# Kernel optimization log

Measured on AMD Instinct MI355X. Metric: run time of the kernel, lower is better.

## Reference

```python
import jax, jax.numpy as jnp
import numpy as np

NUM_HEADS = 8
AREA = 4
EPS = 1e-5  # torch BatchNorm2d default


def _conv1x1(x, w):
    # x: [B,C,H,W], w: [O,C] -> [B,O,H,W]
    return jnp.einsum('bchw,oc->bohw', x, w)


def _bn(y, g, b, m, v):
    # inference-mode BatchNorm2d, per-channel affine
    s = g / jnp.sqrt(v + EPS)
    return y * s[None, :, None, None] + (b - m * s)[None, :, None, None]


def setup_inputs() -> dict:
    key = jax.random.key(0)
    ks = jax.random.split(key, 16)
    B, C, H, W = 2, 256, 64, 64
    d = {}
    d['x'] = jax.random.normal(ks[0], (B, C, H, W), jnp.float32)
    # qk conv (dim -> 2*dim) + BN
    d['w_qk'] = jax.random.normal(ks[1], (2 * C, C), jnp.float32) * 0.06
    d['g_qk'] = jax.random.uniform(ks[2], (2 * C,), jnp.float32, 0.5, 1.5)
    d['b_qk'] = jax.random.normal(ks[3], (2 * C,), jnp.float32) * 0.1
    d['m_qk'] = jax.random.normal(ks[4], (2 * C,), jnp.float32) * 0.1
    d['v_qk'] = jax.random.uniform(ks[5], (2 * C,), jnp.float32, 0.5, 1.5)
    # v conv (dim -> dim) + BN
    d['w_v'] = jax.random.normal(ks[6], (C, C), jnp.float32) * 0.06
    d['g_v'] = jax.random.uniform(ks[7], (C,), jnp.float32, 0.5, 1.5)
    d['b_v'] = jax.random.normal(ks[8], (C,), jnp.float32) * 0.1
    d['m_v'] = jax.random.normal(ks[9], (C,), jnp.float32) * 0.1
    d['v_v'] = jax.random.uniform(ks[10], (C,), jnp.float32, 0.5, 1.5)
    # proj conv (dim -> dim) + BN
    d['w_p'] = jax.random.normal(ks[11], (C, C), jnp.float32) * 0.06
    d['g_p'] = jax.random.uniform(ks[12], (C,), jnp.float32, 0.5, 1.5)
    d['b_p'] = jax.random.normal(ks[13], (C,), jnp.float32) * 0.1
    d['m_p'] = jax.random.normal(ks[14], (C,), jnp.float32) * 0.1
    d['v_p'] = jax.random.uniform(ks[15], (C,), jnp.float32, 0.5, 1.5)
    return d


def reference(x, w_qk, g_qk, b_qk, m_qk, v_qk,
              w_v, g_v, b_v, m_v, v_v,
              w_p, g_p, b_p, m_p, v_p):
    B, C, H, W = x.shape
    N = H * W
    hd = C // NUM_HEADS

    qk = _bn(_conv1x1(x, w_qk), g_qk, b_qk, m_qk, v_qk)          # [B,2C,H,W]
    qk = qk.reshape(B, 2 * C, N).transpose(0, 2, 1)               # [B,N,2C]
    vv = _bn(_conv1x1(x, w_v), g_v, b_v, m_v, v_v)                # [B,C,H,W]
    vv = vv.reshape(B, C, N).transpose(0, 2, 1)                   # [B,N,C]

    Ba, Na = B * AREA, N // AREA
    qk = qk.reshape(Ba, Na, 2 * C)
    vv = vv.reshape(Ba, Na, C)
    q, k = qk[..., :C], qk[..., C:]

    # [Ba,Na,C] -> [Ba,heads,hd,Na] (matches torch transpose(1,2).view)
    q = q.reshape(Ba, Na, NUM_HEADS, hd).transpose(0, 2, 3, 1)
    k = k.reshape(Ba, Na, NUM_HEADS, hd).transpose(0, 2, 3, 1)
    v = vv.reshape(Ba, Na, NUM_HEADS, hd).transpose(0, 2, 3, 1)

    scale = hd ** -0.5
    attn = jnp.einsum('bhdi,bhdj->bhij', q, k) * scale            # [Ba,h,Na,Na]
    attn = jax.nn.softmax(attn, axis=-1)                          # max-sub exp/sum
    out = jnp.einsum('bhdj,bhij->bihd', v, attn)                  # [Ba,Na,h,hd]

    out = out.reshape(B, N, C).reshape(B, H, W, C).transpose(0, 3, 1, 2)
    return _bn(_conv1x1(out, w_p), g_p, b_p, m_p, v_p)            # [B,C,H,W]
```

## Files before the change

kernel.cpp:

```cpp
#include <hip/hip_runtime.h>
#include <hip/hip_bf16.h>
#include <math.h>

#define CCH   256
#define NPIX  4096
#define NHD   8
#define HD    32
#define NA    1024
#define BN_EPS 1e-5f
#define ATT_SCALE (0.17677669529663687f * 1.4426950408889634f)

typedef __attribute__((ext_vector_type(8))) short bf16x8;
typedef __attribute__((ext_vector_type(4))) short bf16x4;
typedef __attribute__((ext_vector_type(4))) float f32x4;

static __device__ inline short f2bf(float f) {
    union { float f; unsigned u; } v; v.f = f;
    unsigned r = (v.u + 0x7fff + ((v.u >> 16) & 1)) >> 16;
    return (short)r;
}

static __device__ inline unsigned int pk2bf(float a, float b) {
    __hip_bfloat162 h2 = __float22bfloat162_rn(make_float2(a, b));
    union { __hip_bfloat162 h; unsigned int u; } v; v.h = h2;
    return v.u;
}

__global__ __launch_bounds__(256)
void prep_kernel(const float* __restrict__ x, short* __restrict__ Xt,
                 const float* __restrict__ wqk, const float* __restrict__ wv,
                 const float* __restrict__ wp, short* __restrict__ Wb) {
    __shared__ short tile[64][66];
    const int t = threadIdx.x;
    const int z = blockIdx.z;
    if (z == 2) {
        const int id  = blockIdx.y * 64 + blockIdx.x;
        const int idx = (id * 256 + t) * 4;
        const float* src; int off;
        if (idx < 131072)      { src = wqk; off = idx; }
        else if (idx < 196608) { src = wv;  off = idx - 131072; }
        else                   { src = wp;  off = idx - 196608; }
        const float4 v = *(const float4*)(src + off);
        short4 o;
        o.x = f2bf(v.x); o.y = f2bf(v.y); o.z = f2bf(v.z); o.w = f2bf(v.w);
        *(short4*)(Wb + idx) = o;
        return;
    }
    const int n0 = blockIdx.x << 6;
    const int c0 = blockIdx.y << 6;
    const int b  = z;
    const float* xp = x + (((size_t)(b * CCH + c0)) << 12) + n0;
    #pragma unroll
    for (int j = 0; j < 16; ++j) {
        const int lin = (j << 8) + t;
        const int cl = lin >> 6, nl = lin & 63;
        tile[cl][nl] = f2bf(xp[((size_t)cl << 12) + nl]);
    }
    __syncthreads();
    short* xtp = Xt + ((((size_t)b << 12) + n0) << 8) + c0;
    #pragma unroll
    for (int j = 0; j < 16; ++j) {
        const int lin = (j << 8) + t;
        const int nl = lin >> 6, cl = lin & 63;
        xtp[((size_t)nl << 8) + cl] = tile[cl][nl];
    }
}

__global__ __launch_bounds__(256)
void qkv_gemm(const short* __restrict__ Xt, const short* __restrict__ Wb,
              const float* __restrict__ g_qk, const float* __restrict__ b_qk,
              const float* __restrict__ m_qk, const float* __restrict__ v_qk,
              const float* __restrict__ g_v, const float* __restrict__ b_v,
              const float* __restrict__ m_v, const float* __restrict__ v_v,
              short* __restrict__ Qb, short* __restrict__ Kb,
              short* __restrict__ Vb) {
    __shared__ short A_lds[64][72];
    __shared__ short B_lds[64][72];
    const int t    = threadIdx.x;
    const int lane = t & 63;
    const int w    = t >> 6;
    const int c    = lane & 15;
    const int quad = lane >> 4;
    const int wm   = w >> 1;
    const int wn   = w & 1;
    const int m0 = blockIdx.x * 64;
    const int n0 = blockIdx.y * 64;

    const int rowS = t >> 3;
    const int kc   = t & 7;
    const short* gA0 = Xt + (size_t)(m0 + rowS) * 256 + kc * 8;
    const short* gA1 = gA0 + 32 * 256;
    const short* gB0 = Wb + (size_t)(n0 + rowS) * 256 + kc * 8;
    const short* gB1 = gB0 + 32 * 256;
    short* lA0 = &A_lds[rowS][kc * 8];
    short* lA1 = &A_lds[rowS + 32][kc * 8];
    short* lB0 = &B_lds[rowS][kc * 8];
    short* lB1 = &B_lds[rowS + 32][kc * 8];

    f32x4 acc[2][2];
    #pragma unroll
    for (int f = 0; f < 2; ++f)
        #pragma unroll
        for (int g = 0; g < 2; ++g) acc[f][g] = (f32x4){0.f, 0.f, 0.f, 0.f};

    #pragma unroll
    for (int kt = 0; kt < 4; ++kt) {
        const int k0 = kt * 64;
        bf16x8 a0 = *(const bf16x8*)(gA0 + k0);
        bf16x8 a1 = *(const bf16x8*)(gA1 + k0);
        bf16x8 b0 = *(const bf16x8*)(gB0 + k0);
        bf16x8 b1 = *(const bf16x8*)(gB1 + k0);
        if (kt) __syncthreads();
        *(bf16x8*)lA0 = a0;
        *(bf16x8*)lA1 = a1;
        *(bf16x8*)lB0 = b0;
        *(bf16x8*)lB1 = b1;
        __syncthreads();
        #pragma unroll
        for (int s = 0; s < 2; ++s) {
            const int ko = s * 32 + quad * 8;
            bf16x8 af0 = *(const bf16x8*)&A_lds[wm * 32 + c][ko];
            bf16x8 af1 = *(const bf16x8*)&A_lds[wm * 32 + 16 + c][ko];
            bf16x8 bg0 = *(const bf16x8*)&B_lds[wn * 32 + c][ko];
            bf16x8 bg1 = *(const bf16x8*)&B_lds[wn * 32 + 16 + c][ko];
            acc[0][0] = __builtin_amdgcn_mfma_f32_16x16x32_bf16(af0, bg0, acc[0][0], 0, 0, 0);
            acc[0][1] = __builtin_amdgcn_mfma_f32_16x16x32_bf16(af0, bg1, acc[0][1], 0, 0, 0);
            acc[1][0] = __builtin_amdgcn_mfma_f32_16x16x32_bf16(af1, bg0, acc[1][0], 0, 0, 0);
            acc[1][1] = __builtin_amdgcn_mfma_f32_16x16x32_bf16(af1, bg1, acc[1][1], 0, 0, 0);
        }
    }

    const int mw = m0 + wm * 32;
    const int nw = n0 + wn * 32;
    if (n0 < 512) {
        const bool isQ = (n0 < 256);
        short* dst = isQ ? Qb : Kb;
        const float fold = isQ ? ATT_SCALE : 1.0f;
        #pragma unroll
        for (int g = 0; g < 2; ++g) {
            const int o  = nw + g * 16 + c;
            const int cd = o & 255;
            const int h  = cd >> 5;
            const int d  = cd & 31;
            float s    = g_qk[o] * rsqrtf(v_qk[o] + BN_EPS);
            float beta = (b_qk[o] - m_qk[o] * s) * fold;
            s *= fold;
            #pragma unroll
            for (int f = 0; f < 2; ++f) {
                #pragma unroll
                for (int r = 0; r < 4; ++r) {
                    const int row  = mw + f * 16 + (quad << 2) + r;
                    const int pair = (row >> 10) * NHD + h;
                    const int i    = row & 1023;
                    dst[(((size_t)pair << 10) + i) * HD + d] = f2bf(acc[f][g][r] * s + beta);
                }
            }
        }
    } else {
        #pragma unroll
        for (int g = 0; g < 2; ++g) {
            const int c2 = nw + g * 16 + c - 512;
            const int d  = c2 & 31;
            const int hp = c2 >> 5;
            const float s    = g_v[c2] * rsqrtf(v_v[c2] + BN_EPS);
            const float beta = b_v[c2] - m_v[c2] * s;
            #pragma unroll
            for (int f = 0; f < 2; ++f) {
                #pragma unroll
                for (int r = 0; r < 4; ++r) {
                    const int row  = mw + f * 16 + (quad << 2) + r;
                    const int pair = (row >> 10) * NHD + hp;
                    const int j    = row & 1023;
                    Vb[((size_t)pair << 15) + (d << 10) + j] = f2bf(acc[f][g][r] * s + beta);
                }
            }
        }
    }
}

__global__ __launch_bounds__(256, 4)
void attn_kernel(const short* __restrict__ Qb,
                 const short* __restrict__ Kb,
                 const short* __restrict__ Vb,
                 short* __restrict__ AOt) {
    const int tid  = threadIdx.x;
    const int wave = tid >> 6;
    const int lane = tid & 63;
    const int c    = lane & 15;
    const int quad = lane >> 4;
    const int pidx  = wave >> 1;
    const int jhalf = wave & 1;

    const int bx  = blockIdx.x;
    const int hi  = bx >> 3;
    const int p   = (bx & 7) + ((hi >> 4) << 3);
    const int blk = hi & 15;
    const int i0a = (blk << 6) + (pidx << 5);
    const int i0b = i0a + 16;
    const int ba  = p >> 3;
    const int h   = p & 7;

    __shared__ f32x4 mrgA[2][4][64];
    __shared__ float mrgL[2][2][64];

    const short* qbase = Qb + ((size_t)p << 15);
    const short* kbase = Kb + ((size_t)p << 15);
    const short* vbase = Vb + ((size_t)p << 15);

    bf16x8 qfa = *(const bf16x8*)(qbase + ((i0a + c) << 5) + (quad << 3));
    bf16x8 qfb = *(const bf16x8*)(qbase + ((i0b + c) << 5) + (quad << 3));

    const int perm = ((c >> 2) << 3) + (c & 3);
    const short* kp0 = kbase + (perm << 5) + (quad << 3);
    const short* kp1 = kp0 + 128;
    const short* vp0 = vbase + (c << 10) + (quad << 3);
    const short* vp1 = vbase + ((c + 16) << 10) + (quad << 3);

    f32x4 acc0a = {0.f,0.f,0.f,0.f}, acc1a = {0.f,0.f,0.f,0.f};
    f32x4 acc0b = {0.f,0.f,0.f,0.f}, acc1b = {0.f,0.f,0.f,0.f};
    float la = 0.f, lb = 0.f;
    const f32x4 zero = {0.f,0.f,0.f,0.f};

    const int jbeg = jhalf << 9;
    for (int jj = 0; jj < 512; jj += 32) {
        const int j0 = jbeg + jj;
        bf16x8 kf0 = *(const bf16x8*)(kp0 + (j0 << 5));
        bf16x8 kf1 = *(const bf16x8*)(kp1 + (j0 << 5));
        bf16x8 vf0 = *(const bf16x8*)(vp0 + j0);
        bf16x8 vf1 = *(const bf16x8*)(vp1 + j0);

        f32x4 s0a = __builtin_amdgcn_mfma_f32_16x16x32_bf16(kf0, qfa, zero, 0, 0, 0);
        f32x4 s1a = __builtin_amdgcn_mfma_f32_16x16x32_bf16(kf1, qfa, zero, 0, 0, 0);
        f32x4 s0b = __builtin_amdgcn_mfma_f32_16x16x32_bf16(kf0, qfb, zero, 0, 0, 0);
        f32x4 s1b = __builtin_amdgcn_mfma_f32_16x16x32_bf16(kf1, qfb, zero, 0, 0, 0);

        float p0a[4], p1a[4], p0b[4], p1b[4];
        #pragma unroll
        for (int r = 0; r < 4; ++r) {
            p0a[r] = __builtin_amdgcn_exp2f(s0a[r]);
            p1a[r] = __builtin_amdgcn_exp2f(s1a[r]);
            p0b[r] = __builtin_amdgcn_exp2f(s0b[r]);
            p1b[r] = __builtin_amdgcn_exp2f(s1b[r]);
        }
        la += (p0a[0]+p0a[1]) + (p0a[2]+p0a[3]) + (p1a[0]+p1a[1]) + (p1a[2]+p1a[3]);
        lb += (p0b[0]+p0b[1]) + (p0b[2]+p0b[3]) + (p1b[0]+p1b[1]) + (p1b[2]+p1b[3]);

        union { unsigned int u[4]; bf16x8 v; } pfa, pfb;
        pfa.u[0] = pk2bf(p0a[0], p0a[1]);
        pfa.u[1] = pk2bf(p0a[2], p0a[3]);
        pfa.u[2] = pk2bf(p1a[0], p1a[1]);
        pfa.u[3] = pk2bf(p1a[2], p1a[3]);
        pfb.u[0] = pk2bf(p0b[0], p0b[1]);
        pfb.u[1] = pk2bf(p0b[2], p0b[3]);
        pfb.u[2] = pk2bf(p1b[0], p1b[1]);
        pfb.u[3] = pk2bf(p1b[2], p1b[3]);

        acc0a = __builtin_amdgcn_mfma_f32_16x16x32_bf16(pfa.v, vf0, acc0a, 0, 0, 0);
        acc1a = __builtin_amdgcn_mfma_f32_16x16x32_bf16(pfa.v, vf1, acc1a, 0, 0, 0);
        acc0b = __builtin_amdgcn_mfma_f32_16x16x32_bf16(pfb.v, vf0, acc0b, 0, 0, 0);
        acc1b = __builtin_amdgcn_mfma_f32_16x16x32_bf16(pfb.v, vf1, acc1b, 0, 0, 0);
    }

    if (jhalf == 1) {
        mrgA[pidx][0][lane] = acc0a;
        mrgA[pidx][1][lane] = acc1a;
        mrgA[pidx][2][lane] = acc0b;
        mrgA[pidx][3][lane] = acc1b;
        mrgL[pidx][0][lane] = la;
        mrgL[pidx][1][lane] = lb;
    }
    __syncthreads();
    if (jhalf == 1) return;

    acc0a += mrgA[pidx][0][lane];
    acc1a += mrgA[pidx][1][lane];
    acc0b += mrgA[pidx][2][lane];
    acc1b += mrgA[pidx][3][lane];
    la += mrgL[pidx][0][lane];
    lb += mrgL[pidx][1][lane];

    la += __shfl_xor(la, 16); la += __shfl_xor(la, 32);
    lb += __shfl_xor(lb, 16); lb += __shfl_xor(lb, 32);

    #pragma unroll
    for (int r = 0; r < 4; ++r) {
        const int rr = (quad << 2) + r;
        const float rla = 1.f / __shfl(la, rr, 16);
        const float rlb = 1.f / __shfl(lb, rr, 16);
        const size_t basea = ((((size_t)ba << 10) + i0a + rr) << 8) + (h << 5);
        const size_t baseb = ((((size_t)ba << 10) + i0b + rr) << 8) + (h << 5);
        AOt[basea + c]      = f2bf(acc0a[r] * rla);
        AOt[basea + c + 16] = f2bf(acc1a[r] * rla);
        AOt[baseb + c]      = f2bf(acc0b[r] * rlb);
        AOt[baseb + c + 16] = f2bf(acc1b[r] * rlb);
    }
}

__global__ __launch_bounds__(256)
void pconv_gemm(const short* __restrict__ Wp, const short* __restrict__ AOt,
                const float* __restrict__ g_p, const float* __restrict__ b_p,
                const float* __restrict__ m_p, const float* __restrict__ v_p,
                float* __restrict__ out) {
    __shared__ short A_lds[64][72];
    __shared__ short B_lds[64][72];
    const int t    = threadIdx.x;
    const int lane = t & 63;
    const int w    = t >> 6;
    const int c    = lane & 15;
    const int quad = lane >> 4;
    const int wm   = w >> 1;
    const int wn   = w & 1;
    const int m0 = blockIdx.x * 64;
    const int n0 = blockIdx.y * 64;

    const int rowS = t >> 3;
    const int kc   = t & 7;
    const short* gA0 = Wp + (size_t)(m0 + rowS) * 256 + kc * 8;
    const short* gA1 = gA0 + 32 * 256;
    const short* gB0 = AOt + (size_t)(n0 + rowS) * 256 + kc * 8;
    const short* gB1 = gB0 + 32 * 256;
    short* lA0 = &A_lds[rowS][kc * 8];
    short* lA1 = &A_lds[rowS + 32][kc * 8];
    short* lB0 = &B_lds[rowS][kc * 8];
    short* lB1 = &B_lds[rowS + 32][kc * 8];

    f32x4 acc[2][2];
    #pragma unroll
    for (int f = 0; f < 2; ++f)
        #pragma unroll
        for (int g = 0; g < 2; ++g) acc[f][g] = (f32x4){0.f, 0.f, 0.f, 0.f};

    #pragma unroll
    for (int kt = 0; kt < 4; ++kt) {
        const int k0 = kt * 64;
        bf16x8 a0 = *(const bf16x8*)(gA0 + k0);
        bf16x8 a1 = *(const bf16x8*)(gA1 + k0);
        bf16x8 b0 = *(const bf16x8*)(gB0 + k0);
        bf16x8 b1 = *(const bf16x8*)(gB1 + k0);
        if (kt) __syncthreads();
        *(bf16x8*)lA0 = a0;
        *(bf16x8*)lA1 = a1;
        *(bf16x8*)lB0 = b0;
        *(bf16x8*)lB1 = b1;
        __syncthreads();
        #pragma unroll
        for (int s = 0; s < 2; ++s) {
            const int ko = s * 32 + quad * 8;
            bf16x8 af0 = *(const bf16x8*)&A_lds[wm * 32 + c][ko];
            bf16x8 af1 = *(const bf16x8*)&A_lds[wm * 32 + 16 + c][ko];
            bf16x8 bg0 = *(const bf16x8*)&B_lds[wn * 32 + c][ko];
            bf16x8 bg1 = *(const bf16x8*)&B_lds[wn * 32 + 16 + c][ko];
            acc[0][0] = __builtin_amdgcn_mfma_f32_16x16x32_bf16(af0, bg0, acc[0][0], 0, 0, 0);
            acc[0][1] = __builtin_amdgcn_mfma_f32_16x16x32_bf16(af0, bg1, acc[0][1], 0, 0, 0);
            acc[1][0] = __builtin_amdgcn_mfma_f32_16x16x32_bf16(af1, bg0, acc[1][0], 0, 0, 0);
            acc[1][1] = __builtin_amdgcn_mfma_f32_16x16x32_bf16(af1, bg1, acc[1][1], 0, 0, 0);
        }
    }

    const int mw = m0 + wm * 32;
    const int nw = n0 + wn * 32;
    #pragma unroll
    for (int f = 0; f < 2; ++f) {
        #pragma unroll
        for (int r = 0; r < 4; ++r) {
            const int o = mw + f * 16 + (quad << 2) + r;
            const float s    = g_p[o] * rsqrtf(v_p[o] + BN_EPS);
            const float beta = b_p[o] - m_p[o] * s;
            #pragma unroll
            for (int g = 0; g < 2; ++g) {
                const int col = nw + g * 16 + c;
                const int b = col >> 12, n = col & 4095;
                out[((size_t)(b * CCH + o) << 12) + n] = acc[f][g][r] * s + beta;
            }
        }
    }
}

extern "C" void kernel_launch(void* const* d_in, const int* in_sizes, int n_in,
                              void* d_out, int out_size, void* d_ws, size_t ws_size,
                              hipStream_t stream) {
    const float* x    = (const float*)d_in[0];
    const float* w_qk = (const float*)d_in[1];
    const float* g_qk = (const float*)d_in[2];
    const float* b_qk = (const float*)d_in[3];
    const float* m_qk = (const float*)d_in[4];
    const float* v_qk = (const float*)d_in[5];
    const float* w_v  = (const float*)d_in[6];
    const float* g_v  = (const float*)d_in[7];
    const float* b_v  = (const float*)d_in[8];
    const float* m_v  = (const float*)d_in[9];
    const float* v_v  = (const float*)d_in[10];
    const float* w_p  = (const float*)d_in[11];
    const float* g_p  = (const float*)d_in[12];
    const float* b_p  = (const float*)d_in[13];
    const float* m_p  = (const float*)d_in[14];
    const float* v_p  = (const float*)d_in[15];

    short* Qb  = (short*)d_ws;
    short* Kb  = Qb + 2097152;
    short* Vb  = Kb + 2097152;
    short* Xt  = Vb + 2097152;
    short* Wb  = Xt + 2097152;
    short* AOt = Xt;

    dim3 gprep(64, 4, 3);
    prep_kernel<<<gprep, 256, 0, stream>>>(x, Xt, w_qk, w_v, w_p, Wb);

    dim3 gqkv(128, 12);
    qkv_gemm<<<gqkv, 256, 0, stream>>>(Xt, Wb, g_qk, b_qk, m_qk, v_qk,
                                       g_v, b_v, m_v, v_v, Qb, Kb, Vb);

    attn_kernel<<<1024, 256, 0, stream>>>(Qb, Kb, Vb, AOt);

    dim3 gp(4, 128);
    pconv_gemm<<<gp, 256, 0, stream>>>(Wb + 768 * 256, AOt, g_p, b_p, m_p, v_p, (float*)d_out);
}
```

Before: 132.1 us.

## Split attention key range across four waves per 32-row query block

Each block now handles 32 query rows, with all four waves splitting the 1024 keys into quarters. Previously two waves each covered half the keys for 64 rows. The grid doubles to 2048 blocks and launch bounds rise to 6 blocks per SM, aiming at more parallelism and shorter per-wave loops. The cost is a three-way shared-memory merge in which three of four waves idle after the barrier, plus more Q reloads and partial-sum traffic.

```diff
diff --git a/kernel.cpp b/kernel.cpp
--- a/kernel.cpp
+++ b/kernel.cpp
@@ -178,7 +178,7 @@
     }
 }
 
-__global__ __launch_bounds__(256, 4)
+__global__ __launch_bounds__(256, 6)
 void attn_kernel(const short* __restrict__ Qb,
                  const short* __restrict__ Kb,
                  const short* __restrict__ Vb,
@@ -188,20 +188,18 @@
     const int lane = tid & 63;
     const int c    = lane & 15;
     const int quad = lane >> 4;
-    const int pidx  = wave >> 1;
-    const int jhalf = wave & 1;
-
-    const int bx  = blockIdx.x;
-    const int hi  = bx >> 3;
-    const int p   = (bx & 7) + ((hi >> 4) << 3);
-    const int blk = hi & 15;
-    const int i0a = (blk << 6) + (pidx << 5);
+
+    const int bx = blockIdx.x;
+    const int hi = bx >> 3;
+    const int p  = ((hi >> 5) << 3) | (bx & 7);
+    const int ig = hi & 31;
+    const int i0a = ig << 5;
     const int i0b = i0a + 16;
     const int ba  = p >> 3;
     const int h   = p & 7;
 
-    __shared__ f32x4 mrgA[2][4][64];
-    __shared__ float mrgL[2][2][64];
+    __shared__ f32x4 mrgA[3][4][64];
+    __shared__ float mrgL[3][2][64];
 
     const short* qbase = Qb + ((size_t)p << 15);
     const short* kbase = Kb + ((size_t)p << 15);
@@ -221,8 +219,8 @@
     float la = 0.f, lb = 0.f;
     const f32x4 zero = {0.f,0.f,0.f,0.f};
 
-    const int jbeg = jhalf << 9;
-    for (int jj = 0; jj < 512; jj += 32) {
+    const int jbeg = wave << 8;
+    for (int jj = 0; jj < 256; jj += 32) {
         const int j0 = jbeg + jj;
         bf16x8 kf0 = *(const bf16x8*)(kp0 + (j0 << 5));
         bf16x8 kf1 = *(const bf16x8*)(kp1 + (j0 << 5));
@@ -261,23 +259,26 @@
         acc1b = __builtin_amdgcn_mfma_f32_16x16x32_bf16(pfb.v, vf1, acc1b, 0, 0, 0);
     }
 
-    if (jhalf == 1) {
-        mrgA[pidx][0][lane] = acc0a;
-        mrgA[pidx][1][lane] = acc1a;
-        mrgA[pidx][2][lane] = acc0b;
-        mrgA[pidx][3][lane] = acc1b;
-        mrgL[pidx][0][lane] = la;
-        mrgL[pidx][1][lane] = lb;
+    if (wave > 0) {
+        mrgA[wave - 1][0][lane] = acc0a;
+        mrgA[wave - 1][1][lane] = acc1a;
+        mrgA[wave - 1][2][lane] = acc0b;
+        mrgA[wave - 1][3][lane] = acc1b;
+        mrgL[wave - 1][0][lane] = la;
+        mrgL[wave - 1][1][lane] = lb;
     }
     __syncthreads();
-    if (jhalf == 1) return;
-
-    acc0a += mrgA[pidx][0][lane];
-    acc1a += mrgA[pidx][1][lane];
-    acc0b += mrgA[pidx][2][lane];
-    acc1b += mrgA[pidx][3][lane];
-    la += mrgL[pidx][0][lane];
-    lb += mrgL[pidx][1][lane];
+    if (wave > 0) return;
+
+    #pragma unroll
+    for (int q = 0; q < 3; ++q) {
+        acc0a += mrgA[q][0][lane];
+        acc1a += mrgA[q][1][lane];
+        acc0b += mrgA[q][2][lane];
+        acc1b += mrgA[q][3][lane];
+        la += mrgL[q][0][lane];
+        lb += mrgL[q][1][lane];
+    }
 
     la += __shfl_xor(la, 16); la += __shfl_xor(la, 32);
     lb += __shfl_xor(lb, 16); lb += __shfl_xor(lb, 32);
@@ -410,7 +411,7 @@
     qkv_gemm<<<gqkv, 256, 0, stream>>>(Xt, Wb, g_qk, b_qk, m_qk, v_qk,
                                        g_v, b_v, m_v, v_v, Qb, Kb, Vb);
 
-    attn_kernel<<<1024, 256, 0, stream>>>(Qb, Kb, Vb, AOt);
+    attn_kernel<<<2048, 256, 0, stream>>>(Qb, Kb, Vb, AOt);
 
     dim3 gp(4, 128);
     pconv_gemm<<<gp, 256, 0, stream>>>(Wb + 768 * 256, AOt, g_p, b_p, m_p, v_p, (float*)d_out);
```

Result: no change. 133.4 us (+0.9%).

## Stage K/V tiles in LDS for attention and enlarge QKV GEMM M-tile

Applied to the files above, without the earlier changes.

The attention kernel now loads K and V tiles for both j-halves into shared memory with coalesced cooperative loads, and applies the row permutation at load time. Before, each wave read K and V fragments straight from global memory. The QKV GEMM moves to a 128-row M-tile so each wave computes 64x32 with 8 accumulators, halving the grid and reusing B fragments more. This adds block-wide syncs in the attention loop and more registers and LDS per block, which could cut occupancy.

```diff
diff --git a/kernel.cpp b/kernel.cpp
--- a/kernel.cpp
+++ b/kernel.cpp
@@ -74,7 +74,7 @@
               const float* __restrict__ m_v, const float* __restrict__ v_v,
               short* __restrict__ Qb, short* __restrict__ Kb,
               short* __restrict__ Vb) {
-    __shared__ short A_lds[64][72];
+    __shared__ short A_lds[128][72];
     __shared__ short B_lds[64][72];
     const int t    = threadIdx.x;
     const int lane = t & 63;
@@ -83,23 +83,27 @@
     const int quad = lane >> 4;
     const int wm   = w >> 1;
     const int wn   = w & 1;
-    const int m0 = blockIdx.x * 64;
-    const int n0 = blockIdx.y * 64;
+    const int m0 = blockIdx.x * 128;
+    const int n0 = blockIdx.y * 64 + wn * 32;
 
     const int rowS = t >> 3;
     const int kc   = t & 7;
     const short* gA0 = Xt + (size_t)(m0 + rowS) * 256 + kc * 8;
     const short* gA1 = gA0 + 32 * 256;
-    const short* gB0 = Wb + (size_t)(n0 + rowS) * 256 + kc * 8;
+    const short* gA2 = gA0 + 64 * 256;
+    const short* gA3 = gA0 + 96 * 256;
+    const short* gB0 = Wb + (size_t)(blockIdx.y * 64 + rowS) * 256 + kc * 8;
     const short* gB1 = gB0 + 32 * 256;
     short* lA0 = &A_lds[rowS][kc * 8];
     short* lA1 = &A_lds[rowS + 32][kc * 8];
+    short* lA2 = &A_lds[rowS + 64][kc * 8];
+    short* lA3 = &A_lds[rowS + 96][kc * 8];
     short* lB0 = &B_lds[rowS][kc * 8];
     short* lB1 = &B_lds[rowS + 32][kc * 8];
 
-    f32x4 acc[2][2];
-    #pragma unroll
-    for (int f = 0; f < 2; ++f)
+    f32x4 acc[4][2];
+    #pragma unroll
+    for (int f = 0; f < 4; ++f)
         #pragma unroll
         for (int g = 0; g < 2; ++g) acc[f][g] = (f32x4){0.f, 0.f, 0.f, 0.f};
 
@@ -108,37 +112,44 @@
         const int k0 = kt * 64;
         bf16x8 a0 = *(const bf16x8*)(gA0 + k0);
         bf16x8 a1 = *(const bf16x8*)(gA1 + k0);
+        bf16x8 a2 = *(const bf16x8*)(gA2 + k0);
+        bf16x8 a3 = *(const bf16x8*)(gA3 + k0);
         bf16x8 b0 = *(const bf16x8*)(gB0 + k0);
         bf16x8 b1 = *(const bf16x8*)(gB1 + k0);
         if (kt) __syncthreads();
         *(bf16x8*)lA0 = a0;
         *(bf16x8*)lA1 = a1;
+        *(bf16x8*)lA2 = a2;
+        *(bf16x8*)lA3 = a3;
         *(bf16x8*)lB0 = b0;
         *(bf16x8*)lB1 = b1;
         __syncthreads();
         #pragma unroll
         for (int s = 0; s < 2; ++s) {
             const int ko = s * 32 + quad * 8;
-            bf16x8 af0 = *(const bf16x8*)&A_lds[wm * 32 + c][ko];
-            bf16x8 af1 = *(const bf16x8*)&A_lds[wm * 32 + 16 + c][ko];
-            bf16x8 bg0 = *(const bf16x8*)&B_lds[wn * 32 + c][ko];
-            bf16x8 bg1 = *(const bf16x8*)&B_lds[wn * 32 + 16 + c][ko];
-            acc[0][0] = __builtin_amdgcn_mfma_f32_16x16x32_bf16(af0, bg0, acc[0][0], 0, 0, 0);
-            acc[0][1] = __builtin_amdgcn_mfma_f32_16x16x32_bf16(af0, bg1, acc[0][1], 0, 0, 0);
-            acc[1][0] = __builtin_amdgcn_mfma_f32_16x16x32_bf16(af1, bg0, acc[1][0], 0, 0, 0);
-            acc[1][1] = __builtin_amdgcn_mfma_f32_16x16x32_bf16(af1, bg1, acc[1][1], 0, 0, 0);
-        }
-    }
-
-    const int mw = m0 + wm * 32;
-    const int nw = n0 + wn * 32;
+            bf16x8 af[4], bg[2];
+            #pragma unroll
+            for (int f = 0; f < 4; ++f)
+                af[f] = *(const bf16x8*)&A_lds[wm * 64 + f * 16 + c][ko];
+            #pragma unroll
+            for (int g = 0; g < 2; ++g)
+                bg[g] = *(const bf16x8*)&B_lds[wn * 32 + g * 16 + c][ko];
+            #pragma unroll
+            for (int f = 0; f < 4; ++f)
+                #pragma unroll
+                for (int g = 0; g < 2; ++g)
+                    acc[f][g] = __builtin_amdgcn_mfma_f32_16x16x32_bf16(af[f], bg[g], acc[f][g], 0, 0, 0);
+        }
+    }
+
+    const int mw = m0 + wm * 64;
     if (n0 < 512) {
         const bool isQ = (n0 < 256);
         short* dst = isQ ? Qb : Kb;
         const float fold = isQ ? ATT_SCALE : 1.0f;
         #pragma unroll
         for (int g = 0; g < 2; ++g) {
-            const int o  = nw + g * 16 + c;
+            const int o  = n0 + g * 16 + c;
             const int cd = o & 255;
             const int h  = cd >> 5;
             const int d  = cd & 31;
@@ -146,7 +157,7 @@
             float beta = (b_qk[o] - m_qk[o] * s) * fold;
             s *= fold;
             #pragma unroll
-            for (int f = 0; f < 2; ++f) {
+            for (int f = 0; f < 4; ++f) {
                 #pragma unroll
                 for (int r = 0; r < 4; ++r) {
                     const int row  = mw + f * 16 + (quad << 2) + r;
@@ -159,13 +170,13 @@
     } else {
         #pragma unroll
         for (int g = 0; g < 2; ++g) {
-            const int c2 = nw + g * 16 + c - 512;
+            const int c2 = n0 + g * 16 + c - 512;
             const int d  = c2 & 31;
             const int hp = c2 >> 5;
             const float s    = g_v[c2] * rsqrtf(v_v[c2] + BN_EPS);
             const float beta = b_v[c2] - m_v[c2] * s;
             #pragma unroll
-            for (int f = 0; f < 2; ++f) {
+            for (int f = 0; f < 4; ++f) {
                 #pragma unroll
                 for (int r = 0; r < 4; ++r) {
                     const int row  = mw + f * 16 + (quad << 2) + r;
@@ -200,6 +211,8 @@
     const int ba  = p >> 3;
     const int h   = p & 7;
 
+    __shared__ __align__(16) short Klds[2][64][40];
+    __shared__ __align__(16) short Vlds[2][32][72];
     __shared__ f32x4 mrgA[2][4][64];
     __shared__ float mrgL[2][2][64];
 
@@ -210,57 +223,80 @@
     bf16x8 qfa = *(const bf16x8*)(qbase + ((i0a + c) << 5) + (quad << 3));
     bf16x8 qfb = *(const bf16x8*)(qbase + ((i0b + c) << 5) + (quad << 3));
 
-    const int perm = ((c >> 2) << 3) + (c & 3);
-    const short* kp0 = kbase + (perm << 5) + (quad << 3);
-    const short* kp1 = kp0 + 128;
-    const short* vp0 = vbase + (c << 10) + (quad << 3);
-    const short* vp1 = vbase + ((c + 16) << 10) + (quad << 3);
+    const int krow = tid >> 2;
+    const int kkc  = tid & 3;
+    const int jj_  = krow >> 5;
+    const int r32  = krow & 31;
+    const int r16  = r32 & 15;
+    const int srcr = ((r16 >> 2) << 3) + (r16 & 3) + ((r32 >> 4) << 2) + (jj_ << 5);
+    const short* kS = kbase + (srcr << 5) + kkc * 8;
+    short* kD0 = &Klds[0][krow][kkc * 8];
+    short* kD1 = &Klds[1][krow][kkc * 8];
+    const int vrow = tid >> 3;
+    const int vkc  = tid & 7;
+    const short* vS = vbase + (vrow << 10) + vkc * 8;
+    short* vD0 = &Vlds[0][vrow][vkc * 8];
+    short* vD1 = &Vlds[1][vrow][vkc * 8];
 
     f32x4 acc0a = {0.f,0.f,0.f,0.f}, acc1a = {0.f,0.f,0.f,0.f};
     f32x4 acc0b = {0.f,0.f,0.f,0.f}, acc1b = {0.f,0.f,0.f,0.f};
     float la = 0.f, lb = 0.f;
     const f32x4 zero = {0.f,0.f,0.f,0.f};
 
-    const int jbeg = jhalf << 9;
-    for (int jj = 0; jj < 512; jj += 32) {
-        const int j0 = jbeg + jj;
-        bf16x8 kf0 = *(const bf16x8*)(kp0 + (j0 << 5));
-        bf16x8 kf1 = *(const bf16x8*)(kp1 + (j0 << 5));
-        bf16x8 vf0 = *(const bf16x8*)(vp0 + j0);
-        bf16x8 vf1 = *(const bf16x8*)(vp1 + j0);
-
-        f32x4 s0a = __builtin_amdgcn_mfma_f32_16x16x32_bf16(kf0, qfa, zero, 0, 0, 0);
-        f32x4 s1a = __builtin_amdgcn_mfma_f32_16x16x32_bf16(kf1, qfa, zero, 0, 0, 0);
-        f32x4 s0b = __builtin_amdgcn_mfma_f32_16x16x32_bf16(kf0, qfb, zero, 0, 0, 0);
-        f32x4 s1b = __builtin_amdgcn_mfma_f32_16x16x32_bf16(kf1, qfb, zero, 0, 0, 0);
-
-        float p0a[4], p1a[4], p0b[4], p1b[4];
-        #pragma unroll
-        for (int r = 0; r < 4; ++r) {
-            p0a[r] = __builtin_amdgcn_exp2f(s0a[r]);
-            p1a[r] = __builtin_amdgcn_exp2f(s1a[r]);
-            p0b[r] = __builtin_amdgcn_exp2f(s0b[r]);
-            p1b[r] = __builtin_amdgcn_exp2f(s1b[r]);
-        }
-        la += (p0a[0]+p0a[1]) + (p0a[2]+p0a[3]) + (p1a[0]+p1a[1]) + (p1a[2]+p1a[3]);
-        lb += (p0b[0]+p0b[1]) + (p0b[2]+p0b[3]) + (p1b[0]+p1b[1]) + (p1b[2]+p1b[3]);
-
-        union { unsigned int u[4]; bf16x8 v; } pfa, pfb;
-        pfa.u[0] = pk2bf(p0a[0], p0a[1]);
-        pfa.u[1] = pk2bf(p0a[2], p0a[3]);
-        pfa.u[2] = pk2bf(p1a[0], p1a[1]);
-        pfa.u[3] = pk2bf(p1a[2], p1a[3]);
-        pfb.u[0] = pk2bf(p0b[0], p0b[1]);
-        pfb.u[1] = pk2bf(p0b[2], p0b[3]);
-        pfb.u[2] = pk2bf(p1b[0], p1b[1]);
-        pfb.u[3] = pk2bf(p1b[2], p1b[3]);
-
-        acc0a = __builtin_amdgcn_mfma_f32_16x16x32_bf16(pfa.v, vf0, acc0a, 0, 0, 0);
-        acc1a = __builtin_amdgcn_mfma_f32_16x16x32_bf16(pfa.v, vf1, acc1a, 0, 0, 0);
-        acc0b = __builtin_amdgcn_mfma_f32_16x16x32_bf16(pfb.v, vf0, acc0b, 0, 0, 0);
-        acc1b = __builtin_amdgcn_mfma_f32_16x16x32_bf16(pfb.v, vf1, acc1b, 0, 0, 0);
-    }
-
+    for (int it = 0; it < 8; ++it) {
+        const int joff = it << 6;
+        bf16x8 k0 = *(const bf16x8*)(kS + (joff << 5));
+        bf16x8 k1 = *(const bf16x8*)(kS + ((joff + 512) << 5));
+        bf16x8 v0 = *(const bf16x8*)(vS + joff);
+        bf16x8 v1 = *(const bf16x8*)(vS + joff + 512);
+        if (it) __syncthreads();
+        *(bf16x8*)kD0 = k0;
+        *(bf16x8*)kD1 = k1;
+        *(bf16x8*)vD0 = v0;
+        *(bf16x8*)vD1 = v1;
+        __syncthreads();
+
+        #pragma unroll
+        for (int jj = 0; jj < 2; ++jj) {
+            bf16x8 kf0 = *(const bf16x8*)&Klds[jhalf][(jj << 5) + c][quad << 3];
+            bf16x8 kf1 = *(const bf16x8*)&Klds[jhalf][(jj << 5) + 16 + c][quad << 3];
+            bf16x8 vf0 = *(const bf16x8*)&Vlds[jhalf][c][(jj << 5) + (quad << 3)];
+            bf16x8 vf1 = *(const bf16x8*)&Vlds[jhalf][c + 16][(jj << 5) + (quad << 3)];
+
+            f32x4 s0a = __builtin_amdgcn_mfma_f32_16x16x32_bf16(kf0, qfa, zero, 0, 0, 0);
+            f32x4 s1a = __builtin_amdgcn_mfma_f32_16x16x32_bf16(kf1, qfa, zero, 0, 0, 0);
+            f32x4 s0b = __builtin_amdgcn_mfma_f32_16x16x32_bf16(kf0, qfb, zero, 0, 0, 0);
+            f32x4 s1b = __builtin_amdgcn_mfma_f32_16x16x32_bf16(kf1, qfb, zero, 0, 0, 0);
+
+            float p0a[4], p1a[4], p0b[4], p1b[4];
+            #pragma unroll
+            for (int r = 0; r < 4; ++r) {
+                p0a[r] = __builtin_amdgcn_exp2f(s0a[r]);
+                p1a[r] = __builtin_amdgcn_exp2f(s1a[r]);
+                p0b[r] = __builtin_amdgcn_exp2f(s0b[r]);
+                p1b[r] = __builtin_amdgcn_exp2f(s1b[r]);
+            }
+            la += (p0a[0]+p0a[1]) + (p0a[2]+p0a[3]) + (p1a[0]+p1a[1]) + (p1a[2]+p1a[3]);
+            lb += (p0b[0]+p0b[1]) + (p0b[2]+p0b[3]) + (p1b[0]+p1b[1]) + (p1b[2]+p1b[3]);
+
+            union { unsigned int u[4]; bf16x8 v; } pfa, pfb;
+            pfa.u[0] = pk2bf(p0a[0], p0a[1]);
+            pfa.u[1] = pk2bf(p0a[2], p0a[3]);
+            pfa.u[2] = pk2bf(p1a[0], p1a[1]);
+            pfa.u[3] = pk2bf(p1a[2], p1a[3]);
+            pfb.u[0] = pk2bf(p0b[0], p0b[1]);
+            pfb.u[1] = pk2bf(p0b[2], p0b[3]);
+            pfb.u[2] = pk2bf(p1b[0], p1b[1]);
+            pfb.u[3] = pk2bf(p1b[2], p1b[3]);
+
+            acc0a = __builtin_amdgcn_mfma_f32_16x16x32_bf16(pfa.v, vf0, acc0a, 0, 0, 0);
+            acc1a = __builtin_amdgcn_mfma_f32_16x16x32_bf16(pfa.v, vf1, acc1a, 0, 0, 0);
+            acc0b = __builtin_amdgcn_mfma_f32_16x16x32_bf16(pfb.v, vf0, acc0b, 0, 0, 0);
+            acc1b = __builtin_amdgcn_mfma_f32_16x16x32_bf16(pfb.v, vf1, acc1b, 0, 0, 0);
+        }
+    }
+
+    __syncthreads();
     if (jhalf == 1) {
         mrgA[pidx][0][lane] = acc0a;
         mrgA[pidx][1][lane] = acc1a;
@@ -406,7 +442,7 @@
     dim3 gprep(64, 4, 3);
     prep_kernel<<<gprep, 256, 0, stream>>>(x, Xt, w_qk, w_v, w_p, Wb);
 
-    dim3 gqkv(128, 12);
+    dim3 gqkv(64, 12);
     qkv_gemm<<<gqkv, 256, 0, stream>>>(Xt, Wb, g_qk, b_qk, m_qk, v_qk,
                                        g_v, b_v, m_v, v_v, Qb, Kb, Vb);
 
```

Result: faster. 123.6 us (-6.4%).
